# Kernel optimization log

Measured on AMD Instinct MI355X. Metric: run time of the kernel, lower is better.

Reference implementation:

```python
import jax, jax.numpy as jnp
import numpy as np

B, CIN, COUT, N, R = 4, 32, 64, 65536, 32
PAD = 0.1
NEG_SLOPE = 0.1


def _norm_coords(coords):
    # coords [B,3,N] in [-1,1]; map to continuous voxel space [0, R-1]
    return jnp.clip((coords / (1.0 + PAD) + 1.0) * 0.5 * (R - 1), 0.0, R - 1)


def scatter_mean(feat, coords):
    # feat [B,C,N], coords [B,3,N] -> voxel grid [B,C,R,R,R]
    b, c, n = feat.shape
    nc = _norm_coords(coords)
    idx = jnp.clip(jnp.floor(nc + 0.5), 0, R - 1).astype(jnp.int32)  # nearest voxel
    flat = (idx[:, 0] * R + idx[:, 1]) * R + idx[:, 2]               # [B,N]
    seg = (flat + jnp.arange(b, dtype=jnp.int32)[:, None] * (R ** 3)).reshape(-1)
    f = feat.transpose(0, 2, 1).reshape(b * n, c)
    sums = jax.ops.segment_sum(f, seg, num_segments=b * R ** 3)
    cnt = jax.ops.segment_sum(jnp.ones((b * n,), feat.dtype), seg, num_segments=b * R ** 3)
    mean = sums / jnp.maximum(cnt, 1.0)[:, None]
    return mean.reshape(b, R, R, R, c).transpose(0, 4, 1, 2, 3)


def trilinear_sample(grid, coords):
    # grid [B,C,R,R,R], coords [B,3,N] -> point features [B,C,N]
    b, c = grid.shape[:2]
    n = coords.shape[-1]
    nc = _norm_coords(coords)                      # [B,3,N]
    lo = jnp.floor(nc).astype(jnp.int32)
    lo = jnp.clip(lo, 0, R - 1)
    hi = jnp.minimum(lo + 1, R - 1)
    frac = nc - lo.astype(nc.dtype)                # [B,3,N]
    gflat = grid.reshape(b, c, R ** 3).transpose(0, 2, 1)  # [B, R^3, C]

    def corner(ix, iy, iz):
        fi = (ix * R + iy) * R + iz                # [B,N]
        return jnp.take_along_axis(gflat, fi[..., None], axis=1)  # [B,N,C]

    fx, fy, fz = frac[:, 0], frac[:, 1], frac[:, 2]
    x0, y0, z0 = lo[:, 0], lo[:, 1], lo[:, 2]
    x1, y1, z1 = hi[:, 0], hi[:, 1], hi[:, 2]
    w = lambda a: a[..., None]
    out = (corner(x0, y0, z0) * w((1 - fx) * (1 - fy) * (1 - fz))
           + corner(x0, y0, z1) * w((1 - fx) * (1 - fy) * fz)
           + corner(x0, y1, z0) * w((1 - fx) * fy * (1 - fz))
           + corner(x0, y1, z1) * w((1 - fx) * fy * fz)
           + corner(x1, y0, z0) * w(fx * (1 - fy) * (1 - fz))
           + corner(x1, y0, z1) * w(fx * (1 - fy) * fz)
           + corner(x1, y1, z0) * w(fx * fy * (1 - fz))
           + corner(x1, y1, z1) * w(fx * fy * fz))
    return out.transpose(0, 2, 1)                  # [B,C,N]


def conv3d(x, w, b):
    y = jax.lax.conv_general_dilated(x, w, (1, 1, 1), 'SAME',
                                     dimension_numbers=('NCDHW', 'OIDHW', 'NCDHW'))
    return y + b[None, :, None, None, None]


def leaky(x):
    return jnp.where(x >= 0, x, NEG_SLOPE * x)


def setup_inputs() -> dict:
    key = jax.random.key(0)
    ks = jax.random.split(key, 6)
    features = jax.random.normal(ks[0], (B, CIN, N), jnp.float32)
    inputs = jax.random.uniform(ks[1], (B, 3, N), jnp.float32) * 2.0 - 1.0  # coords in [-1,1]
    w_mlp = jax.random.normal(ks[2], (COUT, CIN), jnp.float32) * 0.05
    b_mlp = jnp.zeros((COUT,), jnp.float32)
    w_conv1 = jax.random.normal(ks[3], (COUT, CIN, 3, 3, 3), jnp.float32) * 0.05
    b_conv1 = jnp.zeros((COUT,), jnp.float32)
    w_conv2 = jax.random.normal(ks[4], (COUT, COUT, 3, 3, 3), jnp.float32) * 0.05
    b_conv2 = jnp.zeros((COUT,), jnp.float32)
    return {"features": features, "inputs": inputs, "w_mlp": w_mlp, "b_mlp": b_mlp,
            "w_conv1": w_conv1, "b_conv1": b_conv1, "w_conv2": w_conv2, "b_conv2": b_conv2}


def reference(features, inputs, w_mlp, b_mlp, w_conv1, b_conv1, w_conv2, b_conv2):
    # First PVConv layer: voxelize point features (scatter-mean)
    voxel_in = scatter_mean(features, inputs)                     # [B,CIN,R,R,R]
    # point branch: Conv1d(k=1) + ReLU (mlp=False path, norm=None)
    point_feature = jax.nn.relu(jnp.einsum('oc,bcn->bon', w_mlp, features) + b_mlp[None, :, None])
    # voxel branch: DoubleConv = (conv3d -> leaky_relu) x 2, layer_order 'cna' with norm=None
    v = leaky(conv3d(voxel_in, w_conv1, b_conv1))
    voxel_feature = leaky(conv3d(v, w_conv2, b_conv2))            # [B,COUT,R,R,R]
    # fuse point feature: trilinear devoxelization gather + add
    sampled = trilinear_sample(voxel_feature, inputs)             # [B,COUT,N]
    point_out = point_feature + sampled
    return (point_out, voxel_feature)
```

## Files before the change

### kernel.cpp

```cpp
#include <hip/hip_runtime.h>

typedef unsigned short ushort_t;
typedef unsigned int uint_t;
typedef __attribute__((ext_vector_type(4))) float f32x4;
typedef __attribute__((ext_vector_type(4))) unsigned int u32x4;
typedef __attribute__((ext_vector_type(8))) short short8;

#define R3 32768
#define NPTS 65536

__device__ __forceinline__ float bf_lo(uint_t u) { return __uint_as_float(u << 16); }
__device__ __forceinline__ float bf_hi(uint_t u) { return __uint_as_float(u & 0xffff0000u); }
__device__ __forceinline__ ushort_t f2b(float f) {
    uint_t u = __float_as_uint(f);
    u += 0x7fffu + ((u >> 16) & 1u);
    return (ushort_t)(u >> 16);
}
__device__ __forceinline__ float normc(float c) {
    float v = (c / 1.1f + 1.0f) * 0.5f * 31.0f;
    return fminf(fmaxf(v, 0.0f), 31.0f);
}

__global__ __launch_bounds__(256) void k_vid(const float* __restrict__ coords,
                                             int* __restrict__ vid,
                                             uint_t* __restrict__ hist) {
    int gid = blockIdx.x * 256 + threadIdx.x;
    int b = gid >> 16, n = gid & 65535;
    const float* cp = coords + (size_t)b * 3 * NPTS + n;
    int ix = (int)floorf(normc(cp[0]) + 0.5f);
    int iy = (int)floorf(normc(cp[NPTS]) + 0.5f);
    int iz = (int)floorf(normc(cp[2 * NPTS]) + 0.5f);
    ix = min(max(ix, 0), 31); iy = min(max(iy, 0), 31); iz = min(max(iz, 0), 31);
    int v = b * R3 + ((ix * 32 + iy) * 32 + iz);
    vid[gid] = v;
    atomicAdd(hist + v, 1u);
}

__global__ __launch_bounds__(256) void k_scanA(const uint_t* __restrict__ hist,
                                               uint_t* __restrict__ excl,
                                               uint_t* __restrict__ bsum) {
    __shared__ uint_t sh[256];
    int t = threadIdx.x;
    int base = blockIdx.x * 1024 + t * 4;
    uint_t v0 = hist[base], v1 = hist[base + 1], v2 = hist[base + 2], v3 = hist[base + 3];
    uint_t s = v0 + v1 + v2 + v3;
    sh[t] = s;
    __syncthreads();
    uint_t x = s;
    for (int off = 1; off < 256; off <<= 1) {
        uint_t y = (t >= off) ? sh[t - off] : 0u;
        __syncthreads();
        x += y;
        sh[t] = x;
        __syncthreads();
    }
    uint_t e = x - s;
    excl[base] = e;
    excl[base + 1] = e + v0;
    excl[base + 2] = e + v0 + v1;
    excl[base + 3] = e + v0 + v1 + v2;
    if (t == 255) bsum[blockIdx.x] = x;
}

__global__ __launch_bounds__(128) void k_scanB(uint_t* __restrict__ bsum,
                                               uint_t* __restrict__ boff) {
    __shared__ uint_t sh[128];
    int t = threadIdx.x;
    uint_t s = bsum[t];
    sh[t] = s;
    __syncthreads();
    uint_t x = s;
    for (int off = 1; off < 128; off <<= 1) {
        uint_t y = (t >= off) ? sh[t - off] : 0u;
        __syncthreads();
        x += y;
        sh[t] = x;
        __syncthreads();
    }
    boff[t] = x - s;
}

__global__ __launch_bounds__(256) void k_scanC(uint_t* __restrict__ excl,
                                               const uint_t* __restrict__ boff,
                                               uint_t* __restrict__ cursor) {
    int i = blockIdx.x * 256 + threadIdx.x;
    uint_t v = excl[i] + boff[i >> 10];
    excl[i] = v;
    cursor[i] = v;
}

__global__ __launch_bounds__(256) void k_scatfeat(const float* __restrict__ feat,
                                                  const int* __restrict__ vid,
                                                  uint_t* __restrict__ cursor,
                                                  ushort_t* __restrict__ sorted) {
    int gid = blockIdx.x * 256 + threadIdx.x;
    int b = gid >> 16, n = gid & 65535;
    int v = vid[gid];
    uint_t slot = atomicAdd(cursor + v, 1u);
    const float* f = feat + (size_t)b * 32 * NPTS + n;
    ushort_t* dst = sorted + (size_t)slot * 32;
#pragma unroll
    for (int q = 0; q < 4; ++q) {
        u32x4 val;
#pragma unroll
        for (int j = 0; j < 4; ++j) {
            float a = f[(size_t)(q * 8 + j * 2) * NPTS];
            float c = f[(size_t)(q * 8 + j * 2 + 1) * NPTS];
            val[j] = (uint_t)f2b(a) | ((uint_t)f2b(c) << 16);
        }
        *(u32x4*)(dst + q * 8) = val;
    }
}

__global__ __launch_bounds__(256) void k_reduce(const ushort_t* __restrict__ sorted,
                                                const uint_t* __restrict__ start,
                                                const uint_t* __restrict__ hist,
                                                ushort_t* __restrict__ mean_cl) {
    int v = blockIdx.x * 256 + threadIdx.x;
    uint_t s = start[v], c = hist[v];
    float acc[32];
#pragma unroll
    for (int i = 0; i < 32; ++i) acc[i] = 0.0f;
    for (uint_t i = 0; i < c; ++i) {
        const u32x4* p = (const u32x4*)(sorted + (size_t)(s + i) * 32);
#pragma unroll
        for (int q = 0; q < 4; ++q) {
            u32x4 val = p[q];
#pragma unroll
            for (int j = 0; j < 4; ++j) {
                acc[q * 8 + j * 2] += bf_lo(val[j]);
                acc[q * 8 + j * 2 + 1] += bf_hi(val[j]);
            }
        }
    }
    float inv = 1.0f / fmaxf((float)c, 1.0f);
    ushort_t* dst = mean_cl + (size_t)v * 32;
#pragma unroll
    for (int q = 0; q < 4; ++q) {
        u32x4 val;
#pragma unroll
        for (int j = 0; j < 4; ++j)
            val[j] = (uint_t)f2b(acc[q * 8 + j * 2] * inv) |
                     ((uint_t)f2b(acc[q * 8 + j * 2 + 1] * inv) << 16);
        *(u32x4*)(dst + q * 8) = val;
    }
}

__global__ __launch_bounds__(256) void k_wpack(const float* __restrict__ w1,
                                               const float* __restrict__ w2,
                                               ushort_t* __restrict__ Wp1,
                                               ushort_t* __restrict__ Wp2) {
    int t = blockIdx.x * 256 + threadIdx.x;
    if (t < 55296) {
        int dz = t / 18432, r = t % 18432;
        int kb = r >> 9, o = (r >> 3) & 63, ke = r & 7;
        int k = kb * 8 + ke, ci = k & 31, n9 = k >> 5;
        Wp1[t] = f2b(w1[(o * 32 + ci) * 27 + n9 * 3 + dz]);
    } else if (t < 165888) {
        int u = t - 55296;
        int dz = u / 36864, r = u % 36864;
        int kb = r >> 9, o = (r >> 3) & 63, ke = r & 7;
        int k = kb * 8 + ke, ci = k & 63, n9 = k >> 6;
        Wp2[u] = f2b(w2[(o * 64 + ci) * 27 + n9 * 3 + dz]);
    }
}

template <int CI, bool WRITE_CF>
__global__ __launch_bounds__(256) void k_conv(const ushort_t* __restrict__ in_b16,
                                              const ushort_t* __restrict__ Wp,
                                              const float* __restrict__ bias,
                                              ushort_t* __restrict__ out_cl,
                                              float* __restrict__ out_cf) {
    constexpr int KB = CI * 9 / 8;
    constexpr int CB = CI / 8;
    __shared__ ushort_t A[KB][34][8];
    int tid = threadIdx.x, bid = blockIdx.x;
    int b = bid >> 10, xy = bid & 1023, x = xy >> 5, y = xy & 31;

    for (int e = tid; e < 9 * 32 * CB; e += 256) {
        int cb = e % CB, z = (e / CB) & 31, n9 = e / (CB * 32);
        int gx = x + n9 / 3 - 1, gy = y + n9 % 3 - 1;
        u32x4 val = {0u, 0u, 0u, 0u};
        if ((unsigned)gx < 32u && (unsigned)gy < 32u) {
            int ib = b * R3 + (gx * 32 + gy) * 32 + z;
            val = *(const u32x4*)(in_b16 + (size_t)ib * CI + cb * 8);
        }
        *(u32x4*)(&A[n9 * CB + cb][z + 1][0]) = val;
    }
    for (int e = tid; e < KB * 2; e += 256) {
        u32x4 z4 = {0u, 0u, 0u, 0u};
        *(u32x4*)(&A[e >> 1][(e & 1) ? 33 : 0][0]) = z4;
    }
    __syncthreads();

    int lane = tid & 63, wv = tid >> 6;
    int zr = lane & 15, kq = lane >> 4;
    int o = wv * 16 + (lane & 15);
    f32x4 acc0 = {0.f, 0.f, 0.f, 0.f}, acc1 = {0.f, 0.f, 0.f, 0.f};
    const ushort_t* wpB = Wp + (size_t)o * 8;
#pragma unroll
    for (int dz = 0; dz < 3; ++dz) {
#pragma unroll
        for (int kc = 0; kc < KB / 4; ++kc) {
            int kb = kc * 4 + kq;
            short8 a0 = *(const short8*)(&A[kb][zr + dz][0]);
            short8 a1 = *(const short8*)(&A[kb][16 + zr + dz][0]);
            short8 bw = *(const short8*)(wpB + (size_t)(dz * KB + kb) * 512);
            acc0 = __builtin_amdgcn_mfma_f32_16x16x32_bf16(a0, bw, acc0, 0, 0, 0);
            acc1 = __builtin_amdgcn_mfma_f32_16x16x32_bf16(a1, bw, acc1, 0, 0, 0);
        }
    }
    float bia = bias[o];
    float vals[8];
#pragma unroll
    for (int zt = 0; zt < 2; ++zt)
#pragma unroll
        for (int r = 0; r < 4; ++r) {
            float v = (zt ? acc1[r] : acc0[r]) + bia;
            v = (v >= 0.0f) ? v : 0.1f * v;
            vals[zt * 4 + r] = v;
            int z = zt * 16 + kq * 4 + r;
            out_cl[(size_t)(b * R3 + xy * 32 + z) * 64 + o] = f2b(v);
        }
    if (WRITE_CF) {
        __syncthreads();
        float* Dt = (float*)&A[0][0][0];
#pragma unroll
        for (int zt = 0; zt < 2; ++zt)
#pragma unroll
            for (int r = 0; r < 4; ++r)
                Dt[(zt * 16 + kq * 4 + r) * 64 + o] = vals[zt * 4 + r];
        __syncthreads();
        int oo = tid >> 2, zq = tid & 3;
#pragma unroll
        for (int i = 0; i < 2; ++i) {
            f32x4 tv;
#pragma unroll
            for (int j = 0; j < 4; ++j) tv[j] = Dt[(zq * 8 + i * 4 + j) * 64 + oo];
            *(f32x4*)(&out_cf[(size_t)(b * 64 + oo) * R3 + xy * 32 + zq * 8 + i * 4]) = tv;
        }
    }
}

__global__ __launch_bounds__(256) void k_point(const float* __restrict__ feat,
                                               const float* __restrict__ coords,
                                               const float* __restrict__ w_mlp,
                                               const float* __restrict__ b_mlp,
                                               const ushort_t* __restrict__ vf,
                                               float* __restrict__ out) {
    __shared__ int vox_s[64][8];
    __shared__ float wgt_s[64][8];
    __shared__ float S[64][65];
    int tid = threadIdx.x;
    int b = blockIdx.x >> 10;
    int p0 = (blockIdx.x & 1023) * 64;

    {
        int p = tid & 63, cpair = tid >> 6;
        const float* cp = coords + (size_t)b * 3 * NPTS + p0 + p;
        float nx = normc(cp[0]), ny = normc(cp[NPTS]), nz = normc(cp[2 * NPTS]);
        int x0 = min(max((int)floorf(nx), 0), 31);
        int y0 = min(max((int)floorf(ny), 0), 31);
        int z0 = min(max((int)floorf(nz), 0), 31);
        float fx = nx - (float)x0, fy = ny - (float)y0, fz = nz - (float)z0;
        int x1 = min(x0 + 1, 31), y1 = min(y0 + 1, 31), z1 = min(z0 + 1, 31);
#pragma unroll
        for (int j = 0; j < 2; ++j) {
            int c = cpair * 2 + j;
            int xi = (c & 4) ? x1 : x0, yi = (c & 2) ? y1 : y0, zi = (c & 1) ? z1 : z0;
            float wc = ((c & 4) ? fx : 1.0f - fx) * ((c & 2) ? fy : 1.0f - fy) *
                       ((c & 1) ? fz : 1.0f - fz);
            vox_s[p][c] = (xi * 32 + yi) * 32 + zi;
            wgt_s[p][c] = wc;
        }
    }
    __syncthreads();

    int lane = tid & 63, wv = tid >> 6;
    {
        const ushort_t* vfb = vf + (size_t)b * R3 * 64 + lane;
        for (int t = 0; t < 16; ++t) {
            int p = wv * 16 + t;
            float s = 0.0f;
#pragma unroll
            for (int c = 0; c < 8; ++c) {
                int vox = vox_s[p][c];
                float wc = wgt_s[p][c];
                uint_t raw = (uint_t)vfb[(size_t)vox * 64];
                s = fmaf(wc, __uint_as_float(raw << 16), s);
            }
            S[p][lane] = s;
        }
    }
    __syncthreads();

    {
        int o0 = __builtin_amdgcn_readfirstlane(wv) * 16;
        const float* fb = feat + (size_t)b * 32 * NPTS + p0 + lane;
        float ft[32];
#pragma unroll
        for (int ci = 0; ci < 32; ++ci) ft[ci] = fb[(size_t)ci * NPTS];
        float* ob = out + ((size_t)b * 64 + o0) * NPTS + p0 + lane;
#pragma unroll
        for (int oi = 0; oi < 16; ++oi) {
            float m = b_mlp[o0 + oi];
            const float* wrow = w_mlp + (size_t)(o0 + oi) * 32;
#pragma unroll
            for (int ci = 0; ci < 32; ++ci) m = fmaf(wrow[ci], ft[ci], m);
            m = fmaxf(m, 0.0f);
            ob[(size_t)oi * NPTS] = m + S[lane][o0 + oi];
        }
    }
}

extern "C" void kernel_launch(void* const* d_in, const int* in_sizes, int n_in,
                              void* d_out, int out_size, void* d_ws, size_t ws_size,
                              hipStream_t stream) {
    const float* feat   = (const float*)d_in[0];
    const float* coords = (const float*)d_in[1];
    const float* w_mlp  = (const float*)d_in[2];
    const float* b_mlp  = (const float*)d_in[3];
    const float* w_c1   = (const float*)d_in[4];
    const float* b_c1   = (const float*)d_in[5];
    const float* w_c2   = (const float*)d_in[6];
    const float* b_c2   = (const float*)d_in[7];

    float* out = (float*)d_out;
    float* point_out = out;
    float* vfeat = out + 16777216;

    ushort_t* sorted  = (ushort_t*)out;
    ushort_t* mean_cl = (ushort_t*)(out + 4194304);
    ushort_t* v_cl    = (ushort_t*)(out + 6291456);
    int*      vid     = (int*)(out + 10485760);
    uint_t*   hist    = (uint_t*)(out + 10747904);
    uint_t*   excl    = (uint_t*)(out + 10878976);
    uint_t*   cursor  = (uint_t*)(out + 11010048);
    uint_t*   bsum    = (uint_t*)(out + 11141120);
    uint_t*   boff    = (uint_t*)(out + 11141248);
    ushort_t* Wp1     = (ushort_t*)(out + 11141376);
    ushort_t* Wp2     = (ushort_t*)(out + 11169024);
    ushort_t* vf_cl   = (ushort_t*)d_ws;

    hipMemsetAsync(hist, 0, 131072 * 4, stream);
    k_wpack<<<648, 256, 0, stream>>>(w_c1, w_c2, Wp1, Wp2);
    k_vid<<<1024, 256, 0, stream>>>(coords, vid, hist);
    k_scanA<<<128, 256, 0, stream>>>(hist, excl, bsum);
    k_scanB<<<1, 128, 0, stream>>>(bsum, boff);
    k_scanC<<<512, 256, 0, stream>>>(excl, boff, cursor);
    k_scatfeat<<<1024, 256, 0, stream>>>(feat, vid, cursor, sorted);
    k_reduce<<<512, 256, 0, stream>>>(sorted, excl, hist, mean_cl);
    k_conv<32, false><<<4096, 256, 0, stream>>>(mean_cl, Wp1, b_c1, v_cl, (float*)nullptr);
    k_conv<64, true><<<4096, 256, 0, stream>>>(v_cl, Wp2, b_c2, vf_cl, vfeat);
    k_point<<<4096, 256, 0, stream>>>(feat, coords, w_mlp, b_mlp, vf_cl, point_out);
}
```

Baseline: 189.3 us.

## Retile 3D conv to 8x16 yz tiles with double-buffered x-plane staging and 32x32 MFMA

Each conv block now computes an 8x16 (y,z) tile for one x column instead of a full z-line. It stages one padded input x-plane at a time into double-buffered shared memory, overlapping the load of the next plane with compute on the current one. The MFMA changes from 16x16x32 to 32x32x16, and the epilogue goes through shared memory so bf16 channel-last and fp32 channel-first outputs are written with wide vector stores. The goal is less redundant halo loading and better reuse per block. In exchange the grid shrinks to 1024 blocks, and the larger accumulators raise register pressure, which may lower occupancy.

Result: faster. 181.6 us (-4.1%).

```diff
diff --git a/kernel.cpp b/kernel.cpp
--- a/kernel.cpp
+++ b/kernel.cpp
@@ -3,6 +3,7 @@
 typedef unsigned short ushort_t;
 typedef unsigned int uint_t;
 typedef __attribute__((ext_vector_type(4))) float f32x4;
+typedef __attribute__((ext_vector_type(16))) float f32x16;
 typedef __attribute__((ext_vector_type(4))) unsigned int u32x4;
 typedef __attribute__((ext_vector_type(8))) short short8;
 
@@ -165,80 +166,113 @@
     }
 }
 
-template <int CI, bool WRITE_CF>
+template <int CB, bool WRITE_CF>
 __global__ __launch_bounds__(256) void k_conv(const ushort_t* __restrict__ in_b16,
                                               const ushort_t* __restrict__ Wp,
                                               const float* __restrict__ bias,
                                               ushort_t* __restrict__ out_cl,
                                               float* __restrict__ out_cf) {
-    constexpr int KB = CI * 9 / 8;
-    constexpr int CB = CI / 8;
-    __shared__ ushort_t A[KB][34][8];
+    constexpr int CI = CB * 8;
+    constexpr int PLANE_CHUNKS = CB * 10 * 19;
+    __shared__ union ShU {
+        ushort_t T[2][CB][10][19][8];
+        float S[64][132];
+    } sh;
     int tid = threadIdx.x, bid = blockIdx.x;
-    int b = bid >> 10, xy = bid & 1023, x = xy >> 5, y = xy & 31;
-
-    for (int e = tid; e < 9 * 32 * CB; e += 256) {
-        int cb = e % CB, z = (e / CB) & 31, n9 = e / (CB * 32);
-        int gx = x + n9 / 3 - 1, gy = y + n9 % 3 - 1;
-        u32x4 val = {0u, 0u, 0u, 0u};
-        if ((unsigned)gx < 32u && (unsigned)gy < 32u) {
-            int ib = b * R3 + (gx * 32 + gy) * 32 + z;
-            val = *(const u32x4*)(in_b16 + (size_t)ib * CI + cb * 8);
-        }
-        *(u32x4*)(&A[n9 * CB + cb][z + 1][0]) = val;
-    }
-    for (int e = tid; e < KB * 2; e += 256) {
-        u32x4 z4 = {0u, 0u, 0u, 0u};
-        *(u32x4*)(&A[e >> 1][(e & 1) ? 33 : 0][0]) = z4;
-    }
-    __syncthreads();
+    int zh = bid & 1, ys = (bid >> 1) & 3, x = (bid >> 3) & 31, b = bid >> 8;
+    int y0 = ys * 8, z0 = zh * 16;
+
+    auto stage = [&](int dx, int pb) {
+        int gx = x + dx - 1;
+        bool xok = (unsigned)gx < 32u;
+        const ushort_t* src = in_b16 + (size_t)(b * R3 + gx * 1024) * CI;
+        for (int c = tid; c < PLANE_CHUNKS; c += 256) {
+            int zz = c % 19, rem = c / 19;
+            int yy = rem % 10, cb = rem / 10;
+            int gy = y0 + yy - 1, gz = z0 + zz - 1;
+            u32x4 val = {0u, 0u, 0u, 0u};
+            if (xok && (unsigned)gy < 32u && (unsigned)gz < 32u)
+                val = *(const u32x4*)(src + (size_t)(gy * 32 + gz) * CI + cb * 8);
+            *(u32x4*)(&sh.T[pb][cb][yy][zz][0]) = val;
+        }
+    };
 
     int lane = tid & 63, wv = tid >> 6;
-    int zr = lane & 15, kq = lane >> 4;
-    int o = wv * 16 + (lane & 15);
-    f32x4 acc0 = {0.f, 0.f, 0.f, 0.f}, acc1 = {0.f, 0.f, 0.f, 0.f};
-    const ushort_t* wpB = Wp + (size_t)o * 8;
-#pragma unroll
-    for (int dz = 0; dz < 3; ++dz) {
-#pragma unroll
-        for (int kc = 0; kc < KB / 4; ++kc) {
-            int kb = kc * 4 + kq;
-            short8 a0 = *(const short8*)(&A[kb][zr + dz][0]);
-            short8 a1 = *(const short8*)(&A[kb][16 + zr + dz][0]);
-            short8 bw = *(const short8*)(wpB + (size_t)(dz * KB + kb) * 512);
-            acc0 = __builtin_amdgcn_mfma_f32_16x16x32_bf16(a0, bw, acc0, 0, 0, 0);
-            acc1 = __builtin_amdgcn_mfma_f32_16x16x32_bf16(a1, bw, acc1, 0, 0, 0);
-        }
-    }
+    int nq = wv & 1, mq = wv >> 1;
+    int l31 = lane & 31, lh = lane >> 5;
+    int o = nq * 32 + l31;
+    int ya0 = mq * 4 + (l31 >> 4);
+    int ya1 = ya0 + 2;
+    int za = l31 & 15;
+
+    f32x16 acc0, acc1;
+#pragma unroll
+    for (int i = 0; i < 16; ++i) { acc0[i] = 0.0f; acc1[i] = 0.0f; }
+
+    stage(0, 0);
+    __syncthreads();
+#pragma unroll
+    for (int dx = 0; dx < 3; ++dx) {
+        if (dx < 2) stage(dx + 1, (dx + 1) & 1);
+        const ushort_t* Tp = &sh.T[dx & 1][0][0][0][0];
+        const ushort_t* wpB = Wp + (size_t)o * 8;
+#pragma unroll
+        for (int dz = 0; dz < 3; ++dz)
+#pragma unroll
+            for (int dy = 0; dy < 3; ++dy)
+#pragma unroll
+                for (int cbp = 0; cbp < CB / 2; ++cbp) {
+                    int cb = cbp * 2 + lh;
+                    const ushort_t* tb = Tp + (size_t)cb * 10 * 19 * 8;
+                    short8 a0 = *(const short8*)(tb + ((ya0 + dy) * 19 + za + dz) * 8);
+                    short8 a1 = *(const short8*)(tb + ((ya1 + dy) * 19 + za + dz) * 8);
+                    int kb = (dx * 3 + dy) * CB + cb;
+                    short8 bw = *(const short8*)(wpB + (size_t)(dz * 9 * CB + kb) * 512);
+                    acc0 = __builtin_amdgcn_mfma_f32_32x32x16_bf16(a0, bw, acc0, 0, 0, 0);
+                    acc1 = __builtin_amdgcn_mfma_f32_32x32x16_bf16(a1, bw, acc1, 0, 0, 0);
+                }
+        __syncthreads();
+    }
+
     float bia = bias[o];
-    float vals[8];
-#pragma unroll
-    for (int zt = 0; zt < 2; ++zt)
-#pragma unroll
-        for (int r = 0; r < 4; ++r) {
-            float v = (zt ? acc1[r] : acc0[r]) + bia;
-            v = (v >= 0.0f) ? v : 0.1f * v;
-            vals[zt * 4 + r] = v;
-            int z = zt * 16 + kq * 4 + r;
-            out_cl[(size_t)(b * R3 + xy * 32 + z) * 64 + o] = f2b(v);
-        }
+#pragma unroll
+    for (int i = 0; i < 2; ++i) {
+        int mbase = (mq * 2 + i) * 32 + lh * 4;
+#pragma unroll
+        for (int rq = 0; rq < 4; ++rq) {
+            f32x4 v4;
+#pragma unroll
+            for (int j = 0; j < 4; ++j) {
+                float v = (i ? acc1[rq * 4 + j] : acc0[rq * 4 + j]) + bia;
+                v4[j] = (v >= 0.0f) ? v : 0.1f * v;
+            }
+            *(f32x4*)(&sh.S[o][mbase + rq * 8]) = v4;
+        }
+    }
+    __syncthreads();
+
+    {
+        int vl = tid >> 1, oh = tid & 1;
+        int y = vl >> 4, z = vl & 15;
+        ushort_t* dst =
+            out_cl + ((size_t)(b * R3 + x * 1024 + (y0 + y) * 32 + z0 + z)) * 64 + oh * 32;
+#pragma unroll
+        for (int q = 0; q < 4; ++q) {
+            u32x4 w;
+#pragma unroll
+            for (int j4 = 0; j4 < 4; ++j4) {
+                int oo = oh * 32 + q * 8 + j4 * 2;
+                w[j4] = (uint_t)f2b(sh.S[oo][vl]) | ((uint_t)f2b(sh.S[oo + 1][vl]) << 16);
+            }
+            *(u32x4*)(dst + q * 8) = w;
+        }
+    }
     if (WRITE_CF) {
-        __syncthreads();
-        float* Dt = (float*)&A[0][0][0];
-#pragma unroll
-        for (int zt = 0; zt < 2; ++zt)
-#pragma unroll
-            for (int r = 0; r < 4; ++r)
-                Dt[(zt * 16 + kq * 4 + r) * 64 + o] = vals[zt * 4 + r];
-        __syncthreads();
         int oo = tid >> 2, zq = tid & 3;
-#pragma unroll
-        for (int i = 0; i < 2; ++i) {
-            f32x4 tv;
-#pragma unroll
-            for (int j = 0; j < 4; ++j) tv[j] = Dt[(zq * 8 + i * 4 + j) * 64 + oo];
-            *(f32x4*)(&out_cf[(size_t)(b * 64 + oo) * R3 + xy * 32 + zq * 8 + i * 4]) = tv;
-        }
+        float* dp = out_cf + (size_t)(b * 64 + oo) * R3 + x * 1024 + y0 * 32 + z0 + zq * 4;
+#pragma unroll
+        for (int y = 0; y < 8; ++y)
+            *(f32x4*)(dp + y * 32) = *(const f32x4*)(&sh.S[oo][y * 16 + zq * 4]);
     }
 }
 
@@ -350,7 +384,7 @@
     k_scanC<<<512, 256, 0, stream>>>(excl, boff, cursor);
     k_scatfeat<<<1024, 256, 0, stream>>>(feat, vid, cursor, sorted);
     k_reduce<<<512, 256, 0, stream>>>(sorted, excl, hist, mean_cl);
-    k_conv<32, false><<<4096, 256, 0, stream>>>(mean_cl, Wp1, b_c1, v_cl, (float*)nullptr);
-    k_conv<64, true><<<4096, 256, 0, stream>>>(v_cl, Wp2, b_c2, vf_cl, vfeat);
+    k_conv<4, false><<<1024, 256, 0, stream>>>(mean_cl, Wp1, b_c1, v_cl, (float*)nullptr);
+    k_conv<8, true><<<1024, 256, 0, stream>>>(v_cl, Wp2, b_c2, vf_cl, vfeat);
     k_point<<<4096, 256, 0, stream>>>(feat, coords, w_mlp, b_mlp, vf_cl, point_out);
 }
```
